# Kernel tuning notes

Measured on AMD Instinct MI355X. Metric: run time of the kernel, lower is better.

The kernel has to match this reference:

```python
import jax, jax.numpy as jnp
import numpy as np

EPS = 1e-07
B, N, L, K = 256, 512, 4, 1

def setup_inputs() -> dict:
    key = jax.random.key(0)
    k1, k2, k3, k4 = jax.random.split(key, 4)
    x = jax.random.randint(k1, (B, N), 0, L)
    W = jax.random.normal(k2, (N, N), dtype=jnp.float32)
    V_compress = jax.random.normal(k3, (N, L), dtype=jnp.float32)
    E_compress = jax.random.normal(k4, (K, N, N, L, L), dtype=jnp.float32)
    return {"x": x, "W": W, "V_compress": V_compress, "E_compress": E_compress}

def reference(x, W, V_compress, E_compress):
    n = W.shape[0]
    # V: per-variable marginals via softmax over classes
    V = jax.nn.softmax(V_compress, axis=1)                      # (n, l)
    # E: pairwise joints for mixture 0, normalized over (l, l)
    E = jnp.exp(E_compress[0])                                   # (n, n, l, l)
    E = E / E.sum(axis=(-2, -1), keepdims=True)
    A_b = V[:, None, :, None]                                    # row target marginals
    B_b = V[None, :, None, :]                                    # col target marginals
    # IPFP: 2 iterations of row/col marginal rescaling
    for _ in range(2):
        E = E * (A_b / E.sum(axis=3, keepdims=True))
        E = E * (B_b / E.sum(axis=2, keepdims=True))
        E = E / E.sum(axis=(-2, -1), keepdims=True)
    # zero the diagonal blocks and clamp
    E_mask = (1.0 - jnp.eye(n, dtype=E.dtype))[:, :, None, None]
    E = jnp.clip(E * E_mask, 0.0, 1.0)
    # symmetric edge-weight matrix from W
    Ws = jax.nn.sigmoid(W)
    Ws = jnp.tril(Ws, -1)
    Ws = Ws.T + Ws
    L_0 = -Ws + jnp.diag(Ws.sum(axis=1))                         # (n, n)
    # gather per-sample marginals and pairwise joints
    idx = jnp.arange(n)
    Pr = V[idx[None, :], x]                                      # (B, n): Pr[b,i] = V[i, x[b,i]]
    P = E[idx[:, None], idx[None, :], x[:, :, None], x[:, None, :]]  # (B, n, n)
    P = P / (Pr[:, :, None] * Pr[:, None, :])
    WP = Ws[None, :, :] * P                                      # (B, n, n)
    Lap = -WP + jnp.eye(n, dtype=WP.dtype)[None] * WP.sum(axis=2)[:, :, None]
    # matrix-tree: logdet of the (n-1)x(n-1) minor
    _, ld = jnp.linalg.slogdet(Lap[:, 1:, 1:] + EPS)
    _, ld0 = jnp.linalg.slogdet(L_0[1:, 1:] + EPS)
    y = jnp.log(Pr + EPS).sum(axis=1) + ld - ld0                 # (B,)
    return y
```

## Files before the change

### kernel.cpp

```cpp
#include <hip/hip_runtime.h>

#define NN 512
#define NR 511
#define NB 64
#define BATCH 256
#define NMAT 257
#define EPSF 1e-7f
#define NN2 ((size_t)NN * NN)

__device__ __forceinline__ float block_reduce_sum_512(float v, float* red) {
#pragma unroll
  for (int off = 32; off > 0; off >>= 1) v += __shfl_down(v, off, 64);
  int tid = threadIdx.x;
  if ((tid & 63) == 0) red[tid >> 6] = v;
  __syncthreads();
  float s = 0.f;
#pragma unroll
  for (int w = 0; w < 8; ++w) s += red[w];
  return s;
}

__global__ void k_softmaxV(const float* __restrict__ Vc, float* __restrict__ V) {
  int i = threadIdx.x;
  float v0 = Vc[i * 4 + 0], v1 = Vc[i * 4 + 1], v2 = Vc[i * 4 + 2], v3 = Vc[i * 4 + 3];
  float mx = fmaxf(fmaxf(v0, v1), fmaxf(v2, v3));
  float e0 = expf(v0 - mx), e1 = expf(v1 - mx), e2 = expf(v2 - mx), e3 = expf(v3 - mx);
  float s = e0 + e1 + e2 + e3;
  V[i * 4 + 0] = e0 / s; V[i * 4 + 1] = e1 / s; V[i * 4 + 2] = e2 / s; V[i * 4 + 3] = e3 / s;
}

__global__ void k_Ws(const float* __restrict__ W, float* __restrict__ Ws) {
  int i = blockIdx.x, j = threadIdx.x;
  float v = 0.f;
  if (i != j) {
    int hi = i > j ? i : j, lo = i > j ? j : i;
    float wv = W[hi * NN + lo];
    v = 1.f / (1.f + expf(-wv));
  }
  Ws[i * NN + j] = v;
}

__global__ void k_E(const float* __restrict__ Ec, const float* __restrict__ V,
                    float* __restrict__ E) {
  int idx = blockIdx.x * blockDim.x + threadIdx.x;
  if (idx >= NN * NN) return;
  int i = idx >> 9, j = idx & 511;
  float e[16];
  const float* src = Ec + (size_t)idx * 16;
#pragma unroll
  for (int t = 0; t < 16; ++t) e[t] = expf(src[t]);
  float tot = 0.f;
#pragma unroll
  for (int t = 0; t < 16; ++t) tot += e[t];
  float rt = 1.f / tot;
#pragma unroll
  for (int t = 0; t < 16; ++t) e[t] *= rt;
  float Vi[4], Vj[4];
#pragma unroll
  for (int a = 0; a < 4; ++a) { Vi[a] = V[i * 4 + a]; Vj[a] = V[j * 4 + a]; }
#pragma unroll
  for (int it = 0; it < 2; ++it) {
#pragma unroll
    for (int a = 0; a < 4; ++a) {
      float rs = e[a * 4 + 0] + e[a * 4 + 1] + e[a * 4 + 2] + e[a * 4 + 3];
      float sc = Vi[a] / rs;
#pragma unroll
      for (int b = 0; b < 4; ++b) e[a * 4 + b] *= sc;
    }
#pragma unroll
    for (int b = 0; b < 4; ++b) {
      float cs = e[0 + b] + e[4 + b] + e[8 + b] + e[12 + b];
      float sc = Vj[b] / cs;
#pragma unroll
      for (int a = 0; a < 4; ++a) e[a * 4 + b] *= sc;
    }
    float t2 = 0.f;
#pragma unroll
    for (int t = 0; t < 16; ++t) t2 += e[t];
    float rt2 = 1.f / t2;
#pragma unroll
    for (int t = 0; t < 16; ++t) e[t] *= rt2;
  }
  bool diag = (i == j);
#pragma unroll
  for (int t = 0; t < 16; ++t) {
    float v = diag ? 0.f : e[t];
    E[(size_t)t * NN2 + idx] = fminf(fmaxf(v, 0.f), 1.f);
  }
}

__global__ __launch_bounds__(512)
void k_Pr(const int* __restrict__ x, const float* __restrict__ V,
          float* __restrict__ rPr, float* __restrict__ logPr) {
  __shared__ float red[8];
  int b = blockIdx.x, i = threadIdx.x;
  int xi = x[b * NN + i];
  float pr = V[i * 4 + xi];
  rPr[b * NN + i] = 1.f / pr;
  float s = block_reduce_sum_512(logf(pr + EPSF), red);
  if (i == 0) logPr[b] = s;
}

__global__ __launch_bounds__(512)
void k_build(const int* __restrict__ x, const float* __restrict__ Ws,
             const float* __restrict__ E, const float* __restrict__ rPr,
             float* __restrict__ mats, int m0) {
  int slot = blockIdx.y;
  int m = m0 + slot;
  float* A = mats + (size_t)slot * NN2;
  int wv = threadIdx.x >> 6, lane = threadIdx.x & 63;
  int r = blockIdx.x * 8 + wv;
  int jA = lane * 4;
  int jB = 256 + lane * 4;
  float* dstA = A + (size_t)r * NN + jA;
  float* dstB = A + (size_t)r * NN + jB;
  if (r == NR) {
    float4 z = {0.f, 0.f, 0.f, 0.f};
    float4 z1 = {0.f, 0.f, 0.f, 0.f};
    if (lane == 63) z1.w = 1.f;
    *(float4*)dstA = z;
    *(float4*)dstB = z1;
    return;
  }
  int i = r + 1;
  float4 wsA = *(const float4*)&Ws[i * NN + jA];
  float4 wsB = *(const float4*)&Ws[i * NN + jB];
  float wpA[4], wpB[4];
  if (m < BATCH) {
    const int* xm = x + (size_t)m * NN;
    int xi = xm[i];
    int4 xa = *(const int4*)&xm[jA];
    int4 xb = *(const int4*)&xm[jB];
    const float* rp = rPr + (size_t)m * NN;
    float rpi = rp[i];
    float4 ra = *(const float4*)&rp[jA];
    float4 rb = *(const float4*)&rp[jB];
    const float* EbA = E + (size_t)(xi * 4) * NN2 + (size_t)i * NN + jA;
    const float* EbB = E + (size_t)(xi * 4) * NN2 + (size_t)i * NN + jB;
    wpA[0] = wsA.x * EbA[(size_t)xa.x * NN2 + 0] * (rpi * ra.x);
    wpA[1] = wsA.y * EbA[(size_t)xa.y * NN2 + 1] * (rpi * ra.y);
    wpA[2] = wsA.z * EbA[(size_t)xa.z * NN2 + 2] * (rpi * ra.z);
    wpA[3] = wsA.w * EbA[(size_t)xa.w * NN2 + 3] * (rpi * ra.w);
    wpB[0] = wsB.x * EbB[(size_t)xb.x * NN2 + 0] * (rpi * rb.x);
    wpB[1] = wsB.y * EbB[(size_t)xb.y * NN2 + 1] * (rpi * rb.y);
    wpB[2] = wsB.z * EbB[(size_t)xb.z * NN2 + 2] * (rpi * rb.z);
    wpB[3] = wsB.w * EbB[(size_t)xb.w * NN2 + 3] * (rpi * rb.w);
  } else {
    wpA[0] = wsA.x; wpA[1] = wsA.y; wpA[2] = wsA.z; wpA[3] = wsA.w;
    wpB[0] = wsB.x; wpB[1] = wsB.y; wpB[2] = wsB.z; wpB[3] = wsB.w;
  }
  float rs = ((wpA[0] + wpA[1]) + (wpA[2] + wpA[3])) +
             ((wpB[0] + wpB[1]) + (wpB[2] + wpB[3]));
#pragma unroll
  for (int o = 32; o > 0; o >>= 1) rs += __shfl_xor(rs, o, 64);
  float nxtA = __shfl(wpA[0], lane + 1, 64);
  float bndB = __shfl(wpB[0], 0, 64);
  float nxtB = __shfl(wpB[0], lane + 1, 64);
  float shA[4] = {wpA[1], wpA[2], wpA[3], (lane == 63) ? bndB : nxtA};
  float shB[4] = {wpB[1], wpB[2], wpB[3], nxtB};
  float4 oA, oB;
  {
    float o0[4], o1[4];
#pragma unroll
    for (int t = 0; t < 4; ++t) {
      int c = jA + t;
      float v = -shA[t] + EPSF;
      if (c == r) v += rs;
      o0[t] = v;
    }
#pragma unroll
    for (int t = 0; t < 4; ++t) {
      int c = jB + t;
      float v = -shB[t] + EPSF;
      if (c == r) v += rs;
      if (c == NR) v = 0.f;
      o1[t] = v;
    }
    oA = {o0[0], o0[1], o0[2], o0[3]};
    oB = {o1[0], o1[1], o1[2], o1[3]};
  }
  *(float4*)dstA = oA;
  *(float4*)dstB = oB;
}

template <int S>
struct PStepF {
  static __device__ __forceinline__ void run(float (&rr)[64], float (*Prow)[64],
                                             bool own, int tid, float& lgsum) {
    float rinv = 1.f / Prow[S & 1][S];
    if (own && tid > S) {
      float l = rr[S] * rinv;
      rr[S] = l;
      constexpr int C0 = S + 1;
      constexpr int A4 = (C0 + 3) & ~3;
#pragma unroll
      for (int c = C0; c < (A4 < 64 ? A4 : 64); ++c)
        rr[c] = fmaf(-l, Prow[S & 1][c], rr[c]);
#pragma unroll
      for (int g = A4 / 4; g < 16; ++g) {
        float4 u = *(const float4*)&Prow[S & 1][g * 4];
        rr[g * 4 + 0] = fmaf(-l, u.x, rr[g * 4 + 0]);
        rr[g * 4 + 1] = fmaf(-l, u.y, rr[g * 4 + 1]);
        rr[g * 4 + 2] = fmaf(-l, u.z, rr[g * 4 + 2]);
        rr[g * 4 + 3] = fmaf(-l, u.w, rr[g * 4 + 3]);
      }
    }
    if (S + 1 < 64) {
      if (tid == S + 1) {
        lgsum += logf(rr[S + 1]);
#pragma unroll
        for (int c4 = (S + 1) >> 2; c4 < 16; ++c4) {
          float4 v = {rr[c4 * 4 + 0], rr[c4 * 4 + 1], rr[c4 * 4 + 2], rr[c4 * 4 + 3]};
          *(float4*)&Prow[(S + 1) & 1][c4 * 4] = v;
        }
      }
    }
    __syncthreads();
    PStepF<S + 1>::run(rr, Prow, own, tid, lgsum);
  }
};
template <>
struct PStepF<64> {
  static __device__ __forceinline__ void run(float (&)[64], float (*)[64],
                                             bool, int, float&) {}
};

template <int Q>
struct UStep {
  static __device__ __forceinline__ void run(float (&a)[64], const float* L) {
    constexpr int j0 = Q * 4;
    a[j0 + 1] = fmaf(-L[(j0 + 1) * 68 + j0], a[j0], a[j0 + 1]);
    a[j0 + 2] = fmaf(-L[(j0 + 2) * 68 + j0], a[j0], a[j0 + 2]);
    a[j0 + 2] = fmaf(-L[(j0 + 2) * 68 + j0 + 1], a[j0 + 1], a[j0 + 2]);
    a[j0 + 3] = fmaf(-L[(j0 + 3) * 68 + j0], a[j0], a[j0 + 3]);
    a[j0 + 3] = fmaf(-L[(j0 + 3) * 68 + j0 + 1], a[j0 + 1], a[j0 + 3]);
    a[j0 + 3] = fmaf(-L[(j0 + 3) * 68 + j0 + 2], a[j0 + 2], a[j0 + 3]);
#pragma unroll
    for (int t = j0 + 4; t < 64; ++t) {
      float4 Lv = *(const float4*)&L[t * 68 + j0];
      float v = a[t];
      v = fmaf(-Lv.x, a[j0 + 0], v);
      v = fmaf(-Lv.y, a[j0 + 1], v);
      v = fmaf(-Lv.z, a[j0 + 2], v);
      v = fmaf(-Lv.w, a[j0 + 3], v);
      a[t] = v;
    }
    UStep<Q + 1>::run(a, L);
  }
};
template <>
struct UStep<16> {
  static __device__ __forceinline__ void run(float (&)[64], const float*) {}
};

__global__ __launch_bounds__(512)
void k_pu(float* __restrict__ mats, float* __restrict__ ld, int m0, int p) {
  __shared__ __align__(16) float L11[64 * 68];
  __shared__ __align__(16) float Prow[2][64];
  __shared__ float red[8];
  int slot = blockIdx.x;
  float* A = mats + (size_t)slot * NN2;
  int tid = threadIdx.x;
  int k0 = p * NB;
  int m = NN - k0;
  int w = m - NB;
  bool own = tid < m;
  float* myrow = A + (size_t)(k0 + tid) * NN + k0;
  float lgsum = 0.f;
  float rr[64];

  if (own) {
#pragma unroll
    for (int c4 = 0; c4 < 16; ++c4) {
      float4 v = *(const float4*)(myrow + c4 * 4);
      rr[c4 * 4 + 0] = v.x; rr[c4 * 4 + 1] = v.y;
      rr[c4 * 4 + 2] = v.z; rr[c4 * 4 + 3] = v.w;
    }
  } else {
#pragma unroll
    for (int c = 0; c < 64; ++c) rr[c] = 0.f;
  }
  if (tid == 0) {
    lgsum += logf(rr[0]);
#pragma unroll
    for (int c4 = 0; c4 < 16; ++c4) {
      float4 v = {rr[c4 * 4 + 0], rr[c4 * 4 + 1], rr[c4 * 4 + 2], rr[c4 * 4 + 3]};
      *(float4*)&Prow[0][c4 * 4] = v;
    }
  }
  __syncthreads();
  PStepF<0>::run(rr, Prow, own, tid, lgsum);
  if (own && tid >= 64) {
#pragma unroll
    for (int c4 = 0; c4 < 16; ++c4) {
      float4 v = {rr[c4 * 4 + 0], rr[c4 * 4 + 1], rr[c4 * 4 + 2], rr[c4 * 4 + 3]};
      *(float4*)(myrow + c4 * 4) = v;
    }
  }
  if (tid < 64) {
#pragma unroll
    for (int c4 = 0; c4 < 16; ++c4) {
      float4 v = {rr[c4 * 4 + 0], rr[c4 * 4 + 1], rr[c4 * 4 + 2], rr[c4 * 4 + 3]};
      *(float4*)&L11[tid * 68 + c4 * 4] = v;
    }
  }
  __syncthreads();

  if (w > 0 && tid < w) {
    int col = k0 + NB + tid;
#pragma unroll
    for (int t = 0; t < 64; ++t) rr[t] = A[(size_t)(k0 + t) * NN + col];
    UStep<0>::run(rr, L11);
#pragma unroll
    for (int t = 0; t < 64; ++t) A[(size_t)(k0 + t) * NN + col] = rr[t];
  }

  float s = block_reduce_sum_512(lgsum, red);
  if (tid == 0) {
    int gi = m0 + slot;
    if (p == 0) ld[gi] = s;
    else        ld[gi] += s;
  }
}

__global__ __launch_bounds__(256)
void k_gemm(float* __restrict__ mats, int p) {
  __shared__ __align__(16) float At[64 * 136];
  int k0 = p * NB;
  int w = NN - k0 - NB;
  float* A = mats + (size_t)blockIdx.z * NN2;
  int rb = blockIdx.x * 128, cb = blockIdx.y * 128;
  int tid = threadIdx.x;
#pragma unroll
  for (int it = 0; it < 32; ++it) {
    int idx = tid + it * 256;
    int r = idx >> 6, kk = idx & 63;
    int gr = rb + r;
    float v = 0.f;
    if (gr < w) v = A[(size_t)(k0 + NB + gr) * NN + k0 + kk];
    At[kk * 136 + r] = v;
  }
  __syncthreads();
  int ty = tid >> 4, tx = tid & 15;
  int r0 = ty * 8, c0 = tx * 8;
  int gc0 = k0 + NB + cb + c0;
  bool cok = (cb + c0) < w;
  float acc[8][8];
#pragma unroll
  for (int q = 0; q < 8; ++q)
#pragma unroll
    for (int u = 0; u < 8; ++u) acc[q][u] = 0.f;
  float4 bc0 = {0.f, 0.f, 0.f, 0.f}, bc1 = {0.f, 0.f, 0.f, 0.f};
  float4 bn0 = {0.f, 0.f, 0.f, 0.f}, bn1 = {0.f, 0.f, 0.f, 0.f};
  float4 bf0 = {0.f, 0.f, 0.f, 0.f}, bf1 = {0.f, 0.f, 0.f, 0.f};
  if (cok) {
    const float* Br0 = &A[(size_t)k0 * NN + gc0];
    bc0 = *(const float4*)Br0;
    bc1 = *(const float4*)(Br0 + 4);
    const float* Br1 = &A[(size_t)(k0 + 1) * NN + gc0];
    bn0 = *(const float4*)Br1;
    bn1 = *(const float4*)(Br1 + 4);
    const float* Br2 = &A[(size_t)(k0 + 2) * NN + gc0];
    bf0 = *(const float4*)Br2;
    bf1 = *(const float4*)(Br2 + 4);
  }
#pragma unroll 2
  for (int kk = 0; kk < 64; ++kk) {
    float4 bx0 = {0.f, 0.f, 0.f, 0.f}, bx1 = {0.f, 0.f, 0.f, 0.f};
    if (cok && kk < 61) {
      const float* Br = &A[(size_t)(k0 + kk + 3) * NN + gc0];
      bx0 = *(const float4*)Br;
      bx1 = *(const float4*)(Br + 4);
    }
    float4 a0 = *(const float4*)&At[kk * 136 + r0];
    float4 a1 = *(const float4*)&At[kk * 136 + r0 + 4];
    float la[8] = {a0.x, a0.y, a0.z, a0.w, a1.x, a1.y, a1.z, a1.w};
    float lb[8] = {bc0.x, bc0.y, bc0.z, bc0.w, bc1.x, bc1.y, bc1.z, bc1.w};
#pragma unroll
    for (int q = 0; q < 8; ++q)
#pragma unroll
      for (int u = 0; u < 8; ++u) acc[q][u] = fmaf(la[q], lb[u], acc[q][u]);
    bc0 = bn0; bc1 = bn1;
    bn0 = bf0; bn1 = bf1;
    bf0 = bx0; bf1 = bx1;
  }
  if (!cok) return;
#pragma unroll
  for (int q = 0; q < 8; ++q) {
    int gr = rb + r0 + q;
    if (gr < w) {
      float* dst = &A[(size_t)(k0 + NB + gr) * NN + gc0];
      float4 v0 = *(const float4*)dst;
      float4 v1 = *(const float4*)(dst + 4);
      v0.x -= acc[q][0]; v0.y -= acc[q][1]; v0.z -= acc[q][2]; v0.w -= acc[q][3];
      v1.x -= acc[q][4]; v1.y -= acc[q][5]; v1.z -= acc[q][6]; v1.w -= acc[q][7];
      *(float4*)dst = v0;
      *(float4*)(dst + 4) = v1;
    }
  }
}

__global__ void k_y(const float* __restrict__ logPr, const float* __restrict__ ld,
                    float* __restrict__ y) {
  int b = threadIdx.x;
  if (b < BATCH) y[b] = logPr[b] + ld[b] - ld[BATCH];
}

extern "C" void kernel_launch(void* const* d_in, const int* in_sizes, int n_in,
                              void* d_out, int out_size, void* d_ws, size_t ws_size,
                              hipStream_t stream) {
  const int* x = (const int*)d_in[0];
  const float* W = (const float*)d_in[1];
  const float* Vc = (const float*)d_in[2];
  const float* Ec = (const float*)d_in[3];
  float* out = (float*)d_out;

  char* ws = (char*)d_ws;
  size_t off = 0;
  auto alloc = [&](size_t bytes) -> void* {
    void* pp = ws + off;
    off = (off + bytes + 255) & ~(size_t)255;
    return pp;
  };
  float* V     = (float*)alloc((size_t)NN * 4 * 4);
  float* Wsbuf = (float*)alloc(NN2 * 4);
  float* rPr   = (float*)alloc((size_t)BATCH * NN * 4);
  float* logPr = (float*)alloc((size_t)BATCH * 4);
  float* ld    = (float*)alloc((size_t)NMAT * 4);
  float* E     = (float*)alloc(NN2 * 16 * 4);
  size_t per_mat = NN2 * 4;
  size_t remain = ws_size > off ? ws_size - off : 0;
  int cap = (int)(remain / per_mat);
  if (cap > NMAT) cap = NMAT;
  if (cap < 1) cap = 1;
  float* mats = (float*)(ws + off);

  k_softmaxV<<<1, 512, 0, stream>>>(Vc, V);
  k_Ws<<<NN, NN, 0, stream>>>(W, Wsbuf);
  k_E<<<(NN * NN) / 256, 256, 0, stream>>>(Ec, V, E);
  k_Pr<<<BATCH, NN, 0, stream>>>(x, V, rPr, logPr);

  for (int m0 = 0; m0 < NMAT; m0 += cap) {
    int cnt = NMAT - m0 < cap ? NMAT - m0 : cap;
    dim3 gb(64, cnt);
    k_build<<<gb, 512, 0, stream>>>(x, Wsbuf, E, rPr, mats, m0);
    for (int p = 0; p < 8; ++p) {
      k_pu<<<cnt, 512, 0, stream>>>(mats, ld, m0, p);
      int w = NN - p * NB - NB;
      if (w > 0) {
        int nt = (w + 127) / 128;
        dim3 gg(nt, nt, cnt);
        k_gemm<<<gg, 256, 0, stream>>>(mats, p);
      }
    }
  }
  k_y<<<1, 256, 0, stream>>>(logPr, ld, out);
}
```

Baseline: 1.550 ms.

## Compute L21 panel via inverse of U11 GEMM instead of serial row elimination

The panel kernel now factors only the 64x64 diagonal block, inverts its upper-triangular factor by back substitution, and stores the inverse per matrix. A new kernel then computes the L21 panel below the diagonal as a small GEMM against that inverse, replacing the serial per-row elimination done by up to 512 threads inside one block per matrix. This trades a sequential step for a parallel GEMM, at the cost of an extra launch, an extra workspace buffer, and possibly slightly different numerics from using an explicit triangular inverse.

```diff
diff --git a/kernel.cpp b/kernel.cpp
--- a/kernel.cpp
+++ b/kernel.cpp
@@ -225,6 +225,33 @@
                                              bool, int, float&) {}
 };
 
+template <int R>
+struct BackU {
+  static __device__ __forceinline__ void run(float (&x)[64], const float* L,
+                                             int j) {
+    float acc = (j == R) ? 1.f : 0.f;
+    constexpr int C0 = R + 1;
+    constexpr int A4 = (C0 + 3) & ~3;
+#pragma unroll
+    for (int c = C0; c < (A4 < 64 ? A4 : 64); ++c)
+      acc = fmaf(-L[R * 68 + c], x[c], acc);
+#pragma unroll
+    for (int g = A4 / 4; g < 16; ++g) {
+      float4 u = *(const float4*)&L[R * 68 + g * 4];
+      acc = fmaf(-u.x, x[g * 4 + 0], acc);
+      acc = fmaf(-u.y, x[g * 4 + 1], acc);
+      acc = fmaf(-u.z, x[g * 4 + 2], acc);
+      acc = fmaf(-u.w, x[g * 4 + 3], acc);
+    }
+    x[R] = acc / L[R * 68 + R];
+    BackU<R - 1>::run(x, L, j);
+  }
+};
+template <>
+struct BackU<-1> {
+  static __device__ __forceinline__ void run(float (&)[64], const float*, int) {}
+};
+
 template <int Q>
 struct UStep {
   static __device__ __forceinline__ void run(float (&a)[64], const float* L) {
@@ -254,7 +281,8 @@
 };
 
 __global__ __launch_bounds__(512)
-void k_pu(float* __restrict__ mats, float* __restrict__ ld, int m0, int p) {
+void k_pu(float* __restrict__ mats, float* __restrict__ ld,
+          float* __restrict__ Uinv, int m0, int p) {
   __shared__ __align__(16) float L11[64 * 68];
   __shared__ __align__(16) float Prow[2][64];
   __shared__ float red[8];
@@ -262,14 +290,12 @@
   float* A = mats + (size_t)slot * NN2;
   int tid = threadIdx.x;
   int k0 = p * NB;
-  int m = NN - k0;
-  int w = m - NB;
-  bool own = tid < m;
-  float* myrow = A + (size_t)(k0 + tid) * NN + k0;
+  int w = NN - k0 - NB;
   float lgsum = 0.f;
   float rr[64];
 
-  if (own) {
+  if (tid < 64) {
+    const float* myrow = A + (size_t)(k0 + tid) * NN + k0;
 #pragma unroll
     for (int c4 = 0; c4 < 16; ++c4) {
       float4 v = *(const float4*)(myrow + c4 * 4);
@@ -289,14 +315,7 @@
     }
   }
   __syncthreads();
-  PStepF<0>::run(rr, Prow, own, tid, lgsum);
-  if (own && tid >= 64) {
-#pragma unroll
-    for (int c4 = 0; c4 < 16; ++c4) {
-      float4 v = {rr[c4 * 4 + 0], rr[c4 * 4 + 1], rr[c4 * 4 + 2], rr[c4 * 4 + 3]};
-      *(float4*)(myrow + c4 * 4) = v;
-    }
-  }
+  PStepF<0>::run(rr, Prow, tid < 64, tid, lgsum);
   if (tid < 64) {
 #pragma unroll
     for (int c4 = 0; c4 < 16; ++c4) {
@@ -306,6 +325,12 @@
   }
   __syncthreads();
 
+  if (tid < 64 && w > 0) {
+    BackU<63>::run(rr, L11, tid);
+    float* Ug = Uinv + (size_t)slot * 4096;
+#pragma unroll
+    for (int r = 0; r < 64; ++r) Ug[r * 64 + tid] = rr[r];
+  }
   if (w > 0 && tid < w) {
     int col = k0 + NB + tid;
 #pragma unroll
@@ -320,6 +345,63 @@
     int gi = m0 + slot;
     if (p == 0) ld[gi] = s;
     else        ld[gi] += s;
+  }
+}
+
+__global__ __launch_bounds__(256)
+void k_l21(float* __restrict__ mats, const float* __restrict__ Uinv, int p) {
+  __shared__ __align__(16) float Atk[64 * 132];
+  __shared__ __align__(16) float UiL[64 * 64];
+  int k0 = p * NB;
+  int w = NN - k0 - NB;
+  float* A = mats + (size_t)blockIdx.y * NN2;
+  const float* Ug = Uinv + (size_t)blockIdx.y * 4096;
+  int rb = blockIdx.x * 128;
+  int tid = threadIdx.x;
+#pragma unroll
+  for (int it = 0; it < 32; ++it) {
+    int idx = tid + it * 256;
+    int r = idx >> 6, kk = idx & 63;
+    int gr = rb + r;
+    float v = 0.f;
+    if (gr < w) v = A[(size_t)(k0 + NB + gr) * NN + k0 + kk];
+    Atk[kk * 132 + r] = v;
+  }
+#pragma unroll
+  for (int it = 0; it < 16; ++it) {
+    int idx = tid + it * 256;
+    UiL[idx] = Ug[idx];
+  }
+  __syncthreads();
+  int tx = tid & 7, ty = tid >> 3;
+  int c0 = tx * 8, r0 = ty * 4;
+  float acc[4][8];
+#pragma unroll
+  for (int q = 0; q < 4; ++q)
+#pragma unroll
+    for (int u = 0; u < 8; ++u) acc[q][u] = 0.f;
+#pragma unroll 4
+  for (int kk = 0; kk < 64; ++kk) {
+    float4 a0 = *(const float4*)&Atk[kk * 132 + r0];
+    float4 b0 = *(const float4*)&UiL[kk * 64 + c0];
+    float4 b1 = *(const float4*)&UiL[kk * 64 + c0 + 4];
+    float la[4] = {a0.x, a0.y, a0.z, a0.w};
+    float lb[8] = {b0.x, b0.y, b0.z, b0.w, b1.x, b1.y, b1.z, b1.w};
+#pragma unroll
+    for (int q = 0; q < 4; ++q)
+#pragma unroll
+      for (int u = 0; u < 8; ++u) acc[q][u] = fmaf(la[q], lb[u], acc[q][u]);
+  }
+#pragma unroll
+  for (int q = 0; q < 4; ++q) {
+    int gr = rb + r0 + q;
+    if (gr < w) {
+      float* dst = &A[(size_t)(k0 + NB + gr) * NN + k0 + c0];
+      float4 v0 = {acc[q][0], acc[q][1], acc[q][2], acc[q][3]};
+      float4 v1 = {acc[q][4], acc[q][5], acc[q][6], acc[q][7]};
+      *(float4*)dst = v0;
+      *(float4*)(dst + 4) = v1;
+    }
   }
 }
 
@@ -428,6 +510,7 @@
   float* logPr = (float*)alloc((size_t)BATCH * 4);
   float* ld    = (float*)alloc((size_t)NMAT * 4);
   float* E     = (float*)alloc(NN2 * 16 * 4);
+  float* Uinv  = (float*)alloc((size_t)NMAT * 4096 * 4);
   size_t per_mat = NN2 * 4;
   size_t remain = ws_size > off ? ws_size - off : 0;
   int cap = (int)(remain / per_mat);
@@ -445,9 +528,11 @@
     dim3 gb(64, cnt);
     k_build<<<gb, 512, 0, stream>>>(x, Wsbuf, E, rPr, mats, m0);
     for (int p = 0; p < 8; ++p) {
-      k_pu<<<cnt, 512, 0, stream>>>(mats, ld, m0, p);
+      k_pu<<<cnt, 512, 0, stream>>>(mats, ld, Uinv, m0, p);
       int w = NN - p * NB - NB;
       if (w > 0) {
+        dim3 gl((w + 127) / 128, cnt);
+        k_l21<<<gl, 256, 0, stream>>>(mats, Uinv, p);
         int nt = (w + 127) / 128;
         dim3 gg(nt, nt, cnt);
         k_gemm<<<gg, 256, 0, stream>>>(mats, p);
```

New measurement: 1.920 ms. 23.9% more time.
